# Optimization experiments

Measured on AMD Instinct MI355X. Metric: run time of the kernel, lower is better.

The kernel has to match this reference:

```python
import jax, jax.numpy as jnp
import numpy as np

B, T, D, H, C = 256, 512, 1, 1024, 10
STD = 0.01


def setup_inputs() -> dict:
    key = jax.random.key(0)
    ks = jax.random.split(key, 14)
    n = lambda k, shape: STD * jax.random.normal(k, shape, dtype=jnp.float32)
    return {
        "x": jax.random.normal(ks[0], (B, T), dtype=jnp.float32),
        "w_gx": n(ks[1], (D, H)), "w_gh": n(ks[2], (H, H)), "b_g": jnp.zeros((H,), jnp.float32),
        "w_ix": n(ks[3], (D, H)), "w_ih": n(ks[4], (H, H)), "b_i": jnp.zeros((H,), jnp.float32),
        "w_fx": n(ks[5], (D, H)), "w_fh": n(ks[6], (H, H)), "b_f": jnp.zeros((H,), jnp.float32),
        "w_ox": n(ks[7], (D, H)), "w_oh": n(ks[8], (H, H)), "b_o": jnp.zeros((H,), jnp.float32),
        "w_ph": n(ks[9], (H, C)), "b_p": jnp.zeros((C,), jnp.float32),
    }


def _lstm_forward(x, w_gx, w_gh, b_g, w_ix, w_ih, b_i, w_fx, w_fh, b_f,
                  w_ox, w_oh, b_o, w_ph, b_p):
    h_dim = w_gh.shape[0]
    # Fuse the 4 gate weight matrices into single GEMMs per step (cuDNN-style).
    Wx = jnp.concatenate([w_gx, w_ix, w_fx, w_ox], axis=1)   # [D, 4H]
    Wh = jnp.concatenate([w_gh, w_ih, w_fh, w_oh], axis=1)   # [H, 4H]
    b = jnp.concatenate([b_g, b_i, b_f, b_o])                # [4H]

    xt = jnp.swapaxes(x[:, :, None], 0, 1)  # [T, B, D] with D==1
    batch = x.shape[0]
    h0 = jnp.zeros((batch, h_dim), x.dtype)
    c0 = jnp.zeros((batch, h_dim), x.dtype)

    def step(carry, x_t):
        h, c = carry
        z = x_t @ Wx + h @ Wh + b                 # [B, 4H]
        g = jnp.tanh(z[:, :h_dim])
        i = jax.nn.sigmoid(z[:, h_dim:2 * h_dim])
        f = jax.nn.sigmoid(z[:, 2 * h_dim:3 * h_dim])
        o = jax.nn.sigmoid(z[:, 3 * h_dim:])
        c = g * i + c * f
        h = jnp.tanh(c) * o
        return (h, c), None

    (h, _), _ = jax.lax.scan(step, (h0, c0), xt)
    return jax.nn.softmax(h @ w_ph + b_p, axis=-1)  # [B, C]


def reference(x, w_gx, w_gh, b_g, w_ix, w_ih, b_i, w_fx, w_fh, b_f,
              w_ox, w_oh, b_o, w_ph, b_p):
    return _lstm_forward(x, w_gx, w_gh, b_g, w_ix, w_ih, b_i, w_fx, w_fh, b_f,
                         w_ox, w_oh, b_o, w_ph, b_p)
```

## Files before the change

### kernel.cpp

```cpp
#include <hip/hip_runtime.h>

#define Tt  512
#define Hd  1024
#define Cc  10
#define HBHALF (256 * 1024)

typedef short bf16x8 __attribute__((ext_vector_type(8)));
typedef float f32x4 __attribute__((ext_vector_type(4)));

__device__ __forceinline__ unsigned short f2bf(float f) {
  unsigned u = __builtin_bit_cast(unsigned, f);
  u = (u + 0x7FFFu + ((u >> 16) & 1u)) >> 16;
  return (unsigned short)u;
}
__device__ __forceinline__ float bf2f(unsigned short s) {
  unsigned u = ((unsigned)s) << 16;
  return __builtin_bit_cast(float, u);
}
__device__ __forceinline__ float sigmf_(float z) { return 1.0f / (1.0f + __expf(-z)); }
__device__ __forceinline__ float tanhf_(float z) { return 1.0f - 2.0f / (__expf(2.0f * z) + 1.0f); }

__global__ __launch_bounds__(256) void lstm_prep(
    const float* __restrict__ wgh, const float* __restrict__ wih,
    const float* __restrict__ wfh, const float* __restrict__ woh,
    unsigned short* __restrict__ whT)
{
  __shared__ float tile[64][65];
  const int bid = blockIdx.x;
  const int q  = bid >> 8;
  const int ct = (bid >> 4) & 15;
  const int kt = bid & 15;
  const float* w = (q == 0) ? wgh : (q == 1) ? wih : (q == 2) ? wfh : woh;
  const int tid = threadIdx.x;
  const int tc = tid & 63, tr = tid >> 6;
  #pragma unroll
  for (int i = 0; i < 16; ++i) {
    int kk = i * 4 + tr;
    tile[kk][tc] = w[(size_t)(kt * 64 + kk) * Hd + ct * 64 + tc];
  }
  __syncthreads();
  #pragma unroll
  for (int i = 0; i < 16; ++i) {
    int cc = i * 4 + tr;
    whT[(size_t)(q * 1024 + ct * 64 + cc) * Hd + kt * 64 + tc] = f2bf(tile[tc][cc]);
  }
}

__global__ __launch_bounds__(512) void lstm_step(
    const unsigned short* __restrict__ whT,
    const float* __restrict__ x,
    const float* __restrict__ wgx, const float* __restrict__ wix,
    const float* __restrict__ wfx, const float* __restrict__ wox,
    const float* __restrict__ bg,  const float* __restrict__ bi,
    const float* __restrict__ bfp, const float* __restrict__ bo,
    const unsigned short* __restrict__ hR,
    unsigned short* __restrict__ hW,
    float* __restrict__ cbuf,
    int t)
{
  extern __shared__ char smem[];
  char*  hls  = smem;
  float* zbuf = (float*)(smem + 65536);
  __shared__ float xsh[32];

  const int tid = threadIdx.x;
  const int l   = tid & 63;
  const int w   = tid >> 6;
  const int cb  = blockIdx.x & 31;
  const int rg  = blockIdx.x >> 5;
  const int r0  = rg * 32;
  const int hc0 = cb * 32;

  if (tid < 32) xsh[tid] = x[(size_t)(r0 + tid) * Tt + t];

  {
    int rbase = w * 4;
    #pragma unroll
    for (int i = 0; i < 8; ++i) {
      int r = rbase + (i >> 1);
      int half = i & 1;
      char* ldsb = hls + r * 2048 + half * 1024;
      int m = half * 64 + l;
      int srcc = m ^ (r & 7);
      const char* gp = (const char*)hR + (((size_t)(r0 + r) << 10) + srcc * 8) * 2;
      __builtin_amdgcn_global_load_lds(gp, ldsb, 16, 0, 0);
    }
  }
  __syncthreads();

  const int q  = w >> 1;
  const int lc = l & 15;
  const int roff0 = lc * 2048;
  const int roff1 = roff0 + 16 * 2048;
  const int swz   = (l & 7) << 4;
  const int kboff = (l >> 4) * 16;
  const unsigned short* wcol =
      whT + (size_t)(q * 1024 + hc0 + ((w & 1) << 4) + lc) * Hd + (l >> 4) * 8;

  f32x4 acc0 = {0.f,0.f,0.f,0.f};
  f32x4 acc1 = {0.f,0.f,0.f,0.f};
  #pragma unroll
  for (int kc = 0; kc < 32; ++kc) {
    int boff = (kc * 64 + kboff) ^ swz;
    bf16x8 a0 = *(const bf16x8*)(hls + roff0 + boff);
    bf16x8 a1 = *(const bf16x8*)(hls + roff1 + boff);
    bf16x8 b  = *(const bf16x8*)(wcol + kc * 32);
    acc0 = __builtin_amdgcn_mfma_f32_16x16x32_bf16(a0, b, acc0, 0, 0, 0);
    acc1 = __builtin_amdgcn_mfma_f32_16x16x32_bf16(a1, b, acc1, 0, 0, 0);
  }

  {
    int colz  = (w << 4) + lc;
    int rbase = (l >> 4) * 4;
    #pragma unroll
    for (int p = 0; p < 4; ++p) {
      zbuf[(rbase + p) * 128 + colz]      = acc0[p];
      zbuf[(rbase + p + 16) * 128 + colz] = acc1[p];
    }
  }
  __syncthreads();

  #pragma unroll
  for (int e = 0; e < 2; ++e) {
    int idx = tid + e * 512;
    int r = idx >> 5, hc = idx & 31;
    int hcol = hc0 + hc;
    float xv = xsh[r];
    float zg = zbuf[r * 128 +       hc] + xv * wgx[hcol] + bg[hcol];
    float zi = zbuf[r * 128 +  32 + hc] + xv * wix[hcol] + bi[hcol];
    float zf = zbuf[r * 128 +  64 + hc] + xv * wfx[hcol] + bfp[hcol];
    float zo = zbuf[r * 128 +  96 + hc] + xv * wox[hcol] + bo[hcol];
    float G = tanhf_(zg);
    float I = sigmf_(zi);
    float F = sigmf_(zf);
    float O = sigmf_(zo);
    size_t ci = (size_t)(r0 + r) * Hd + hcol;
    float cnew = G * I + cbuf[ci] * F;
    cbuf[ci] = cnew;
    hW[ci] = f2bf(tanhf_(cnew) * O);
  }
}

__global__ __launch_bounds__(256) void lstm_final(
    const unsigned short* __restrict__ h, const float* __restrict__ wph,
    const float* __restrict__ bp, float* __restrict__ out)
{
  __shared__ float zrow[16][10];
  const int tid = threadIdx.x;
  if (tid < 160) {
    int rr = tid / 10, c = tid - rr * 10;
    int r = blockIdx.x * 16 + rr;
    float acc = bp[c];
    for (int k8 = 0; k8 < 128; ++k8) {
      bf16x8 hv = *(const bf16x8*)(h + (size_t)r * Hd + k8 * 8);
      #pragma unroll
      for (int e = 0; e < 8; ++e)
        acc += bf2f((unsigned short)hv[e]) * wph[(k8 * 8 + e) * Cc + c];
    }
    zrow[rr][c] = acc;
  }
  __syncthreads();
  if (tid < 16) {
    int r = blockIdx.x * 16 + tid;
    float m = -1e30f;
    #pragma unroll
    for (int cc = 0; cc < Cc; ++cc) m = fmaxf(m, zrow[tid][cc]);
    float s = 0.f;
    float ev[Cc];
    #pragma unroll
    for (int cc = 0; cc < Cc; ++cc) { ev[cc] = __expf(zrow[tid][cc] - m); s += ev[cc]; }
    float inv = 1.0f / s;
    #pragma unroll
    for (int cc = 0; cc < Cc; ++cc) out[r * Cc + cc] = ev[cc] * inv;
  }
}

extern "C" void kernel_launch(void* const* d_in, const int* in_sizes, int n_in,
                              void* d_out, int out_size, void* d_ws, size_t ws_size,
                              hipStream_t stream) {
  const float* x   = (const float*)d_in[0];
  const float* wgx = (const float*)d_in[1];
  const float* wgh = (const float*)d_in[2];
  const float* bg  = (const float*)d_in[3];
  const float* wix = (const float*)d_in[4];
  const float* wih = (const float*)d_in[5];
  const float* bi  = (const float*)d_in[6];
  const float* wfx = (const float*)d_in[7];
  const float* wfh = (const float*)d_in[8];
  const float* bfp = (const float*)d_in[9];
  const float* wox = (const float*)d_in[10];
  const float* woh = (const float*)d_in[11];
  const float* bo  = (const float*)d_in[12];
  const float* wph = (const float*)d_in[13];
  const float* bp  = (const float*)d_in[14];
  float* out = (float*)d_out;

  unsigned short* whT  = (unsigned short*)d_ws;
  unsigned short* hbuf = (unsigned short*)((char*)d_ws + (size_t)4 * 1024 * Hd * 2);
  float* cbuf = (float*)((char*)hbuf + (size_t)2 * HBHALF * 2);

  hipMemsetAsync(hbuf, 0, (size_t)HBHALF * 2, stream);
  hipMemsetAsync(cbuf, 0, (size_t)HBHALF * 4, stream);

  hipFuncSetAttribute((const void*)lstm_step,
                      hipFuncAttributeMaxDynamicSharedMemorySize, 81920);

  lstm_prep<<<1024, 256, 0, stream>>>(wgh, wih, wfh, woh, whT);

  for (int t = 0; t < Tt; ++t) {
    const unsigned short* hR = hbuf + (size_t)(t & 1) * HBHALF;
    unsigned short*       hW = hbuf + (size_t)((t + 1) & 1) * HBHALF;
    lstm_step<<<256, 512, 81920, stream>>>(whT, x, wgx, wix, wfx, wox,
                                           bg, bi, bfp, bo, hR, hW, cbuf, t);
  }

  lstm_final<<<16, 256, 0, stream>>>(hbuf , wph, bp, out);
}
```

Baseline: 5.592 ms.

## Run several LSTM timesteps per cooperative launch with grid-wide sync

Replaces the per-timestep kernel launch with a cooperative kernel that loops over 8 timesteps and uses grid.sync() between them, cutting the number of launches by a factor of eight. This targets kernel launch and teardown overhead on the sequential recurrence. In exchange it adds cooperative-launch overhead and grid barrier cost, and it requires all 256 blocks of 512 threads with 80KB LDS to be co-resident.

```diff
diff --git a/kernel.cpp b/kernel.cpp
--- a/kernel.cpp
+++ b/kernel.cpp
@@ -1,9 +1,13 @@
 #include <hip/hip_runtime.h>
+#include <hip/hip_cooperative_groups.h>
+
+namespace cg = cooperative_groups;
 
 #define Tt  512
 #define Hd  1024
 #define Cc  10
 #define HBHALF (256 * 1024)
+#define SSTEPS 8
 
 typedef short bf16x8 __attribute__((ext_vector_type(8)));
 typedef float f32x4 __attribute__((ext_vector_type(4)));
@@ -46,22 +50,23 @@
   }
 }
 
-__global__ __launch_bounds__(512) void lstm_step(
+__global__ __launch_bounds__(512) void lstm_multi(
     const unsigned short* __restrict__ whT,
     const float* __restrict__ x,
     const float* __restrict__ wgx, const float* __restrict__ wix,
     const float* __restrict__ wfx, const float* __restrict__ wox,
     const float* __restrict__ bg,  const float* __restrict__ bi,
     const float* __restrict__ bfp, const float* __restrict__ bo,
-    const unsigned short* __restrict__ hR,
-    unsigned short* __restrict__ hW,
+    unsigned short* __restrict__ hbuf,
     float* __restrict__ cbuf,
-    int t)
+    int t0)
 {
   extern __shared__ char smem[];
   char*  hls  = smem;
   float* zbuf = (float*)(smem + 65536);
   __shared__ float xsh[32];
+
+  cg::grid_group grid = cg::this_grid();
 
   const int tid = threadIdx.x;
   const int l   = tid & 63;
@@ -70,23 +75,6 @@
   const int rg  = blockIdx.x >> 5;
   const int r0  = rg * 32;
   const int hc0 = cb * 32;
-
-  if (tid < 32) xsh[tid] = x[(size_t)(r0 + tid) * Tt + t];
-
-  {
-    int rbase = w * 4;
-    #pragma unroll
-    for (int i = 0; i < 8; ++i) {
-      int r = rbase + (i >> 1);
-      int half = i & 1;
-      char* ldsb = hls + r * 2048 + half * 1024;
-      int m = half * 64 + l;
-      int srcc = m ^ (r & 7);
-      const char* gp = (const char*)hR + (((size_t)(r0 + r) << 10) + srcc * 8) * 2;
-      __builtin_amdgcn_global_load_lds(gp, ldsb, 16, 0, 0);
-    }
-  }
-  __syncthreads();
 
   const int q  = w >> 1;
   const int lc = l & 15;
@@ -97,47 +85,73 @@
   const unsigned short* wcol =
       whT + (size_t)(q * 1024 + hc0 + ((w & 1) << 4) + lc) * Hd + (l >> 4) * 8;
 
-  f32x4 acc0 = {0.f,0.f,0.f,0.f};
-  f32x4 acc1 = {0.f,0.f,0.f,0.f};
-  #pragma unroll
-  for (int kc = 0; kc < 32; ++kc) {
-    int boff = (kc * 64 + kboff) ^ swz;
-    bf16x8 a0 = *(const bf16x8*)(hls + roff0 + boff);
-    bf16x8 a1 = *(const bf16x8*)(hls + roff1 + boff);
-    bf16x8 b  = *(const bf16x8*)(wcol + kc * 32);
-    acc0 = __builtin_amdgcn_mfma_f32_16x16x32_bf16(a0, b, acc0, 0, 0, 0);
-    acc1 = __builtin_amdgcn_mfma_f32_16x16x32_bf16(a1, b, acc1, 0, 0, 0);
-  }
-
-  {
-    int colz  = (w << 4) + lc;
-    int rbase = (l >> 4) * 4;
-    #pragma unroll
-    for (int p = 0; p < 4; ++p) {
-      zbuf[(rbase + p) * 128 + colz]      = acc0[p];
-      zbuf[(rbase + p + 16) * 128 + colz] = acc1[p];
-    }
-  }
-  __syncthreads();
-
-  #pragma unroll
-  for (int e = 0; e < 2; ++e) {
-    int idx = tid + e * 512;
-    int r = idx >> 5, hc = idx & 31;
-    int hcol = hc0 + hc;
-    float xv = xsh[r];
-    float zg = zbuf[r * 128 +       hc] + xv * wgx[hcol] + bg[hcol];
-    float zi = zbuf[r * 128 +  32 + hc] + xv * wix[hcol] + bi[hcol];
-    float zf = zbuf[r * 128 +  64 + hc] + xv * wfx[hcol] + bfp[hcol];
-    float zo = zbuf[r * 128 +  96 + hc] + xv * wox[hcol] + bo[hcol];
-    float G = tanhf_(zg);
-    float I = sigmf_(zi);
-    float F = sigmf_(zf);
-    float O = sigmf_(zo);
-    size_t ci = (size_t)(r0 + r) * Hd + hcol;
-    float cnew = G * I + cbuf[ci] * F;
-    cbuf[ci] = cnew;
-    hW[ci] = f2bf(tanhf_(cnew) * O);
+  #pragma unroll 1
+  for (int s = 0; s < SSTEPS; ++s) {
+    const int t = t0 + s;
+    const unsigned short* hR = hbuf + (size_t)(t & 1) * HBHALF;
+    unsigned short*       hW = hbuf + (size_t)((t + 1) & 1) * HBHALF;
+
+    if (tid < 32) xsh[tid] = x[(size_t)(r0 + tid) * Tt + t];
+
+    {
+      int rbase = w * 4;
+      #pragma unroll
+      for (int i = 0; i < 8; ++i) {
+        int r = rbase + (i >> 1);
+        int half = i & 1;
+        char* ldsb = hls + r * 2048 + half * 1024;
+        int m = half * 64 + l;
+        int srcc = m ^ (r & 7);
+        const char* gp = (const char*)hR + (((size_t)(r0 + r) << 10) + srcc * 8) * 2;
+        __builtin_amdgcn_global_load_lds(gp, ldsb, 16, 0, 0);
+      }
+    }
+    __syncthreads();
+
+    f32x4 acc0 = {0.f,0.f,0.f,0.f};
+    f32x4 acc1 = {0.f,0.f,0.f,0.f};
+    #pragma unroll
+    for (int kc = 0; kc < 32; ++kc) {
+      int boff = (kc * 64 + kboff) ^ swz;
+      bf16x8 a0 = *(const bf16x8*)(hls + roff0 + boff);
+      bf16x8 a1 = *(const bf16x8*)(hls + roff1 + boff);
+      bf16x8 b  = *(const bf16x8*)(wcol + kc * 32);
+      acc0 = __builtin_amdgcn_mfma_f32_16x16x32_bf16(a0, b, acc0, 0, 0, 0);
+      acc1 = __builtin_amdgcn_mfma_f32_16x16x32_bf16(a1, b, acc1, 0, 0, 0);
+    }
+
+    {
+      int colz  = (w << 4) + lc;
+      int rbase = (l >> 4) * 4;
+      #pragma unroll
+      for (int p = 0; p < 4; ++p) {
+        zbuf[(rbase + p) * 128 + colz]      = acc0[p];
+        zbuf[(rbase + p + 16) * 128 + colz] = acc1[p];
+      }
+    }
+    __syncthreads();
+
+    #pragma unroll
+    for (int e = 0; e < 2; ++e) {
+      int idx = tid + e * 512;
+      int r = idx >> 5, hc = idx & 31;
+      int hcol = hc0 + hc;
+      float xv = xsh[r];
+      float zg = zbuf[r * 128 +       hc] + xv * wgx[hcol] + bg[hcol];
+      float zi = zbuf[r * 128 +  32 + hc] + xv * wix[hcol] + bi[hcol];
+      float zf = zbuf[r * 128 +  64 + hc] + xv * wfx[hcol] + bfp[hcol];
+      float zo = zbuf[r * 128 +  96 + hc] + xv * wox[hcol] + bo[hcol];
+      float G = tanhf_(zg);
+      float I = sigmf_(zi);
+      float F = sigmf_(zf);
+      float O = sigmf_(zo);
+      size_t ci = (size_t)(r0 + r) * Hd + hcol;
+      float cnew = G * I + cbuf[ci] * F;
+      cbuf[ci] = cnew;
+      hW[ci] = f2bf(tanhf_(cnew) * O);
+    }
+
+    grid.sync();
   }
 }
 
@@ -202,16 +216,20 @@
   hipMemsetAsync(hbuf, 0, (size_t)HBHALF * 2, stream);
   hipMemsetAsync(cbuf, 0, (size_t)HBHALF * 4, stream);
 
-  hipFuncSetAttribute((const void*)lstm_step,
+  hipFuncSetAttribute((const void*)lstm_multi,
                       hipFuncAttributeMaxDynamicSharedMemorySize, 81920);
 
   lstm_prep<<<1024, 256, 0, stream>>>(wgh, wih, wfh, woh, whT);
 
-  for (int t = 0; t < Tt; ++t) {
-    const unsigned short* hR = hbuf + (size_t)(t & 1) * HBHALF;
-    unsigned short*       hW = hbuf + (size_t)((t + 1) & 1) * HBHALF;
-    lstm_step<<<256, 512, 81920, stream>>>(whT, x, wgx, wix, wfx, wox,
-                                           bg, bi, bfp, bo, hR, hW, cbuf, t);
+  for (int t0 = 0; t0 < Tt; t0 += SSTEPS) {
+    void* args[] = {
+      (void*)&whT, (void*)&x,
+      (void*)&wgx, (void*)&wix, (void*)&wfx, (void*)&wox,
+      (void*)&bg,  (void*)&bi,  (void*)&bfp, (void*)&bo,
+      (void*)&hbuf, (void*)&cbuf, (void*)&t0
+    };
+    hipLaunchCooperativeKernel((const void*)lstm_multi, dim3(256), dim3(512),
+                               args, 81920u, stream);
   }
 
   lstm_final<<<16, 256, 0, stream>>>(hbuf , wph, bp, out);
```

Measured after the change: 18.51 ms. +231.0%, slower.

## Prefetch weights into registers, overlap with h load, special-case first step

Applied to the files above, without the earlier changes.

The step kernel now loads its whole B-operand weight slice into registers, along with the input weight, bias and cell state, before the barrier, so these global loads overlap the async h-to-LDS copy. The x-projection and bias are folded into the MFMA accumulator's initial value instead of being added during the gate epilogue. x is transposed once up front so each step reads a contiguous row. Step 0, where h and c are zero, runs as a cheap elementwise kernel, which also removes the memsets. The register-held weights (32 bf16x8 per thread) raise register pressure, and the launch bound of 2 blocks may force spills.

```diff
diff --git a/kernel.cpp b/kernel.cpp
--- a/kernel.cpp
+++ b/kernel.cpp
@@ -46,9 +46,50 @@
   }
 }
 
-__global__ __launch_bounds__(512) void lstm_step(
+__global__ __launch_bounds__(256) void x_prep(
+    const float* __restrict__ x, float* __restrict__ xT)
+{
+  __shared__ float tile[32][33];
+  const int bx = blockIdx.x & 15;
+  const int by = blockIdx.x >> 4;
+  const int tc = threadIdx.x & 31, tr = threadIdx.x >> 5;
+  #pragma unroll
+  for (int i = 0; i < 4; ++i) {
+    int rr = i * 8 + tr;
+    tile[rr][tc] = x[(size_t)(by * 32 + rr) * Tt + bx * 32 + tc];
+  }
+  __syncthreads();
+  #pragma unroll
+  for (int i = 0; i < 4; ++i) {
+    int tt = i * 8 + tr;
+    xT[(size_t)(bx * 32 + tt) * 256 + by * 32 + tc] = tile[tc][tt];
+  }
+}
+
+__global__ __launch_bounds__(512) void lstm_step0(
+    const float* __restrict__ xT,
+    const float* __restrict__ wgx, const float* __restrict__ wix,
+    const float* __restrict__ wfx, const float* __restrict__ wox,
+    const float* __restrict__ bg,  const float* __restrict__ bi,
+    const float* __restrict__ bfp, const float* __restrict__ bo,
+    unsigned short* __restrict__ h1,
+    float* __restrict__ cbuf)
+{
+  int idx = blockIdx.x * 512 + threadIdx.x;
+  int r = idx >> 10, hc = idx & 1023;
+  float xv = xT[r];
+  float G = tanhf_(xv * wgx[hc] + bg[hc]);
+  float I = sigmf_(xv * wix[hc] + bi[hc]);
+  float O = sigmf_(xv * wox[hc] + bo[hc]);
+  (void)bfp; (void)wfx;
+  float c = G * I;
+  cbuf[idx] = c;
+  h1[idx] = f2bf(tanhf_(c) * O);
+}
+
+__global__ __launch_bounds__(512, 2) void lstm_step(
     const unsigned short* __restrict__ whT,
-    const float* __restrict__ x,
+    const float* __restrict__ xT,
     const float* __restrict__ wgx, const float* __restrict__ wix,
     const float* __restrict__ wfx, const float* __restrict__ wox,
     const float* __restrict__ bg,  const float* __restrict__ bi,
@@ -71,7 +112,7 @@
   const int r0  = rg * 32;
   const int hc0 = cb * 32;
 
-  if (tid < 32) xsh[tid] = x[(size_t)(r0 + tid) * Tt + t];
+  if (tid < 32) xsh[tid] = xT[(size_t)t * 256 + r0 + tid];
 
   {
     int rbase = w * 4;
@@ -86,59 +127,81 @@
       __builtin_amdgcn_global_load_lds(gp, ldsb, 16, 0, 0);
     }
   }
-  __syncthreads();
-
-  const int q  = w >> 1;
-  const int lc = l & 15;
+
+  const int q   = w >> 1;
+  const int lc  = l & 15;
+  const int bcol = hc0 + ((w & 1) << 4) + lc;
+  const unsigned short* wcol = whT + (size_t)(q * 1024 + bcol) * Hd + (l >> 4) * 8;
+  bf16x8 bq[32];
+  #pragma unroll
+  for (int kc = 0; kc < 32; ++kc) bq[kc] = *(const bf16x8*)(wcol + kc * 32);
+
+  const float* wxp = (q == 0) ? wgx : (q == 1) ? wix : (q == 2) ? wfx : wox;
+  const float* bbp = (q == 0) ? bg  : (q == 1) ? bi  : (q == 2) ? bfp : bo;
+  const float wxv = wxp[bcol];
+  const float bbv = bbp[bcol];
+
+  const int r_a = tid >> 5, hc_a = tid & 31;
+  const int r_b = (tid + 512) >> 5;
+  const size_t ci_a = (size_t)(r0 + r_a) * Hd + hc0 + hc_a;
+  const size_t ci_b = (size_t)(r0 + r_b) * Hd + hc0 + hc_a;
+  const float c_a = cbuf[ci_a];
+  const float c_b = cbuf[ci_b];
+
+  __syncthreads();
+
+  const int rb4 = (l >> 4) * 4;
+  f32x4 acc0, acc1;
+  #pragma unroll
+  for (int p = 0; p < 4; ++p) {
+    acc0[p] = bbv + xsh[rb4 + p] * wxv;
+    acc1[p] = bbv + xsh[rb4 + p + 16] * wxv;
+  }
+
   const int roff0 = lc * 2048;
   const int roff1 = roff0 + 16 * 2048;
   const int swz   = (l & 7) << 4;
   const int kboff = (l >> 4) * 16;
-  const unsigned short* wcol =
-      whT + (size_t)(q * 1024 + hc0 + ((w & 1) << 4) + lc) * Hd + (l >> 4) * 8;
-
-  f32x4 acc0 = {0.f,0.f,0.f,0.f};
-  f32x4 acc1 = {0.f,0.f,0.f,0.f};
   #pragma unroll
   for (int kc = 0; kc < 32; ++kc) {
     int boff = (kc * 64 + kboff) ^ swz;
     bf16x8 a0 = *(const bf16x8*)(hls + roff0 + boff);
     bf16x8 a1 = *(const bf16x8*)(hls + roff1 + boff);
-    bf16x8 b  = *(const bf16x8*)(wcol + kc * 32);
-    acc0 = __builtin_amdgcn_mfma_f32_16x16x32_bf16(a0, b, acc0, 0, 0, 0);
-    acc1 = __builtin_amdgcn_mfma_f32_16x16x32_bf16(a1, b, acc1, 0, 0, 0);
-  }
-
-  {
-    int colz  = (w << 4) + lc;
-    int rbase = (l >> 4) * 4;
+    acc0 = __builtin_amdgcn_mfma_f32_16x16x32_bf16(a0, bq[kc], acc0, 0, 0, 0);
+    acc1 = __builtin_amdgcn_mfma_f32_16x16x32_bf16(a1, bq[kc], acc1, 0, 0, 0);
+  }
+
+  {
+    int colz = (w << 4) + lc;
     #pragma unroll
     for (int p = 0; p < 4; ++p) {
-      zbuf[(rbase + p) * 128 + colz]      = acc0[p];
-      zbuf[(rbase + p + 16) * 128 + colz] = acc1[p];
+      zbuf[(rb4 + p) * 128 + colz]      = acc0[p];
+      zbuf[(rb4 + p + 16) * 128 + colz] = acc1[p];
     }
   }
   __syncthreads();
 
-  #pragma unroll
-  for (int e = 0; e < 2; ++e) {
-    int idx = tid + e * 512;
-    int r = idx >> 5, hc = idx & 31;
-    int hcol = hc0 + hc;
-    float xv = xsh[r];
-    float zg = zbuf[r * 128 +       hc] + xv * wgx[hcol] + bg[hcol];
-    float zi = zbuf[r * 128 +  32 + hc] + xv * wix[hcol] + bi[hcol];
-    float zf = zbuf[r * 128 +  64 + hc] + xv * wfx[hcol] + bfp[hcol];
-    float zo = zbuf[r * 128 +  96 + hc] + xv * wox[hcol] + bo[hcol];
-    float G = tanhf_(zg);
-    float I = sigmf_(zi);
-    float F = sigmf_(zf);
-    float O = sigmf_(zo);
-    size_t ci = (size_t)(r0 + r) * Hd + hcol;
-    float cnew = G * I + cbuf[ci] * F;
-    cbuf[ci] = cnew;
-    hW[ci] = f2bf(tanhf_(cnew) * O);
-  }
+  float cn_a, cn_b;
+  {
+    float zg = zbuf[r_a * 128 +       hc_a];
+    float zi = zbuf[r_a * 128 +  32 + hc_a];
+    float zf = zbuf[r_a * 128 +  64 + hc_a];
+    float zo = zbuf[r_a * 128 +  96 + hc_a];
+    float G = tanhf_(zg), I = sigmf_(zi), F = sigmf_(zf), O = sigmf_(zo);
+    cn_a = G * I + c_a * F;
+    hW[ci_a] = f2bf(tanhf_(cn_a) * O);
+  }
+  {
+    float zg = zbuf[r_b * 128 +       hc_a];
+    float zi = zbuf[r_b * 128 +  32 + hc_a];
+    float zf = zbuf[r_b * 128 +  64 + hc_a];
+    float zo = zbuf[r_b * 128 +  96 + hc_a];
+    float G = tanhf_(zg), I = sigmf_(zi), F = sigmf_(zf), O = sigmf_(zo);
+    cn_b = G * I + c_b * F;
+    hW[ci_b] = f2bf(tanhf_(cn_b) * O);
+  }
+  cbuf[ci_a] = cn_a;
+  cbuf[ci_b] = cn_b;
 }
 
 __global__ __launch_bounds__(256) void lstm_final(
@@ -198,19 +261,23 @@
   unsigned short* whT  = (unsigned short*)d_ws;
   unsigned short* hbuf = (unsigned short*)((char*)d_ws + (size_t)4 * 1024 * Hd * 2);
   float* cbuf = (float*)((char*)hbuf + (size_t)2 * HBHALF * 2);
-
-  hipMemsetAsync(hbuf, 0, (size_t)HBHALF * 2, stream);
-  hipMemsetAsync(cbuf, 0, (size_t)HBHALF * 4, stream);
-
+  float* xT   = (float*)((char*)cbuf + (size_t)HBHALF * 4);
+
+  size_t shmem = 65536 + 16384;
   hipFuncSetAttribute((const void*)lstm_step,
-                      hipFuncAttributeMaxDynamicSharedMemorySize, 81920);
+                      hipFuncAttributeMaxDynamicSharedMemorySize, (int)shmem);
 
   lstm_prep<<<1024, 256, 0, stream>>>(wgh, wih, wfh, woh, whT);
-
-  for (int t = 0; t < Tt; ++t) {
+  x_prep<<<128, 256, 0, stream>>>(x, xT);
+
+  lstm_step0<<<512, 512, 0, stream>>>(xT, wgx, wix, wfx, wox,
+                                      bg, bi, bfp, bo,
+                                      hbuf + HBHALF, cbuf);
+
+  for (int t = 1; t < Tt; ++t) {
     const unsigned short* hR = hbuf + (size_t)(t & 1) * HBHALF;
     unsigned short*       hW = hbuf + (size_t)((t + 1) & 1) * HBHALF;
-    lstm_step<<<256, 512, 81920, stream>>>(whT, x, wgx, wix, wfx, wox,
+    lstm_step<<<256, 512, shmem, stream>>>(whT, xT, wgx, wix, wfx, wox,
                                            bg, bi, bfp, bo, hR, hW, cbuf, t);
   }
 
```

After: 6.670 ms. +19.3%, slower.
